# Optimization experiments

Hardware: AMD Instinct MI355X
Metric: run time of the kernel (lower is better)

Reference implementation:

```python
import jax, jax.numpy as jnp
import numpy as np

C = 343.0      # speed of sound (init kwarg c)
F = 16         # number of frequency channels (len(omega))
H = 128        # MLP hidden width
N = 131072     # collocation points


def _mlp(coords, W1, b1, W2, b2, W3, b3):
    # coords: [..., 3] -> [..., 2F] (first F = real part, last F = imag part)
    h = jnp.tanh(coords @ W1 + b1)
    h = jnp.tanh(h @ W2 + b2)
    return h @ W3 + b3


def setup_inputs() -> dict:
    key = jax.random.key(0)
    ks = jax.random.split(key, 4)
    inputs = jax.random.normal(ks[0], (N, 3), dtype=jnp.float32)
    # omega = 2*pi*f for f = 100..1600 Hz (matches init kwarg list)
    omega = 2.0 * jnp.pi * 100.0 * jnp.arange(1, F + 1, dtype=jnp.float32)
    s_in = 1.0 / np.sqrt(3.0)
    s_h = 1.0 / np.sqrt(float(H))
    W1 = jax.random.normal(ks[1], (3, H), dtype=jnp.float32) * s_in
    b1 = jnp.zeros((H,), dtype=jnp.float32)
    W2 = jax.random.normal(ks[2], (H, H), dtype=jnp.float32) * s_h
    b2 = jnp.zeros((H,), dtype=jnp.float32)
    W3 = jax.random.normal(ks[3], (H, 2 * F), dtype=jnp.float32) * s_h
    b3 = jnp.zeros((2 * F,), dtype=jnp.float32)
    return {"inputs": inputs, "omega": omega, "W1": W1, "b1": b1,
            "W2": W2, "b2": b2, "W3": W3, "b3": b3}


def reference(inputs, omega, W1, b1, W2, b2, W3, b3):
    # Pointwise network R^3 -> R^{2F} (real/imag stacked).
    f = lambda c3: _mlp(c3, W1, b1, W2, b2, W3, b3)

    # u: complex pressure per point per frequency, [N, F]
    out = _mlp(inputs, W1, b1, W2, b2, W3, b3)           # [N, 2F]
    u = out[:, :F] + 1j * out[:, F:]

    # Full spatial Hessian per point via forward-over-reverse AD (fused
    # replacement for the torch per-channel autograd.grad loop).
    hess = jax.vmap(jax.jacfwd(jax.jacrev(f)))(inputs)   # [N, 2F, 3, 3]
    lap_ri = jnp.einsum('nfii->nf', hess)                # diagonal trace = Laplacian
    lap = lap_ri[:, :F] + 1j * lap_ri[:, F:]             # [N, F] complex

    # PDE residual skips channel 0, exactly as the torch loop (i+1 indexing).
    k2 = (omega[1:] / C) ** 2                            # [F-1]
    residual = lap[:, 1:] + k2 * u[:, 1:]                # [N, F-1]

    # mean over channels then over batch == global mean of |residual|^2
    return jnp.mean(jnp.abs(residual) ** 2)
```

## Files before the change

kernel.cpp:

```cpp
#include <hip/hip_runtime.h>
#include <math.h>

#ifndef __has_builtin
#define __has_builtin(x) 0
#endif

#define NPTS   131072
#define FCH    16
#define CSND   343.0f
#define PB     16
#define BLOCK  256
#define GRID   512
#define NBLK   (NPTS / PB)

typedef _Float16 half8 __attribute__((ext_vector_type(8)));
typedef _Float16 half2v __attribute__((ext_vector_type(2)));
typedef float    f32x4 __attribute__((ext_vector_type(4)));

static __device__ __forceinline__ unsigned pack2(float a, float b) {
#if __has_builtin(__builtin_amdgcn_cvt_pkrtz)
  return __builtin_bit_cast(unsigned, __builtin_amdgcn_cvt_pkrtz(a, b));
#else
  half2v v; v[0] = (_Float16)a; v[1] = (_Float16)b;
  return __builtin_bit_cast(unsigned, v);
#endif
}

static __device__ __forceinline__ float mytanh(float x) {
  float ax = fabsf(x);
  float e  = __expf(-2.0f * ax);
  float r  = (1.0f - e) * __builtin_amdgcn_rcpf(1.0f + e);
  return copysignf(r, x);
}


__global__ __launch_bounds__(BLOCK, 2) void helmholtz_kernel(
    const float* __restrict__ x,
    const float* __restrict__ omega,
    const float* __restrict__ W1,
    const float* __restrict__ b1,
    const float* __restrict__ W2,
    const float* __restrict__ b2,
    const float* __restrict__ W3,
    const float* __restrict__ b3,
    float* __restrict__ out)
{
  __shared__ unsigned s_A[2][80 * 64];
  __shared__ unsigned s_HG[2][32 * 64];

  const int tid  = threadIdx.x;
  const int w    = tid >> 6;
  const int l    = tid & 63;
  const int col  = l & 15;
  const int quad = l >> 4;

  const int i2 = l;
  const float a0x = W1[2 * i2],     a0y = W1[128 + 2 * i2], a0z = W1[256 + 2 * i2];
  const float a1x = W1[2 * i2 + 1], a1y = W1[129 + 2 * i2], a1z = W1[257 + 2 * i2];
  const float bb0 = b1[2 * i2],     bb1 = b1[2 * i2 + 1];
  const float wsq0 = a0x * a0x + a0y * a0y + a0z * a0z;
  const float wsq1 = a1x * a1x + a1y * a1y + a1z * a1z;

  half8 w2f[2][4];
#pragma unroll
  for (int ntl = 0; ntl < 2; ntl++) {
    const int n = (2 * w + ntl) * 16 + col;
#pragma unroll
    for (int ks = 0; ks < 4; ks++) {
      half8 f;
#pragma unroll
      for (int j = 0; j < 8; j++)
        f[j] = (_Float16)W2[(ks * 32 + (quad << 3) + j) * 128 + n];
      w2f[ntl][ks] = f;
    }
  }
  half8 w3f[4];
  {
    const int n = (w & 1) * 16 + col;
#pragma unroll
    for (int ks = 0; ks < 4; ks++) {
      half8 f;
#pragma unroll
      for (int j = 0; j < 8; j++)
        f[j] = (_Float16)W3[(ks * 32 + (quad << 3) + j) * 32 + n];
      w3f[ks] = f;
    }
  }

  const float b2r0 = b2[2 * w * 16 + col];
  const float b2r1 = b2[(2 * w + 1) * 16 + col];
  float k2v = 0.0f;
  if (col >= 1) {
    float om = omega[col] * (1.0f / CSND);
    k2v = om * om;
  }
  const float b3v = b3[(w & 1) * 16 + col];

  float wsum = 0.0f;

  auto phaseA = [&](int blk, int buf) {
    const int pbase = blk * PB;
    unsigned* sA = s_A[buf];
#pragma unroll
    for (int it = 0; it < 4; it++) {
      int p = w * 4 + it;
      const float* xp = x + (size_t)(pbase + p) * 3;
      float x0 = xp[0], x1 = xp[1], x2 = xp[2];
      float z0 = fmaf(x0, a0x, fmaf(x1, a0y, fmaf(x2, a0z, bb0)));
      float z1 = fmaf(x0, a1x, fmaf(x1, a1y, fmaf(x2, a1z, bb1)));
      float t0 = mytanh(z0), t1 = mytanh(z1);
      float s0 = 1.0f - t0 * t0, s1 = 1.0f - t1 * t1;
      unsigned u_h  = pack2(t0, t1);
      unsigned u_d0 = pack2(s0 * a0x, s1 * a1x);
      unsigned u_d1 = pack2(s0 * a0y, s1 * a1y);
      unsigned u_d2 = pack2(s0 * a0z, s1 * a1z);
      unsigned u_c  = pack2(-2.0f * t0 * s0 * wsq0, -2.0f * t1 * s1 * wsq1);
      int dcol = (((i2 >> 2) ^ p) << 2) + (i2 & 3);
      sA[(p)      * 64 + dcol] = u_h;
      sA[(16 + p) * 64 + dcol] = u_d0;
      sA[(32 + p) * 64 + dcol] = u_d1;
      sA[(48 + p) * 64 + dcol] = u_d2;
      sA[(64 + p) * 64 + dcol] = u_c;
    }
  };

  phaseA(blockIdx.x, 0);
  __syncthreads();

  int parity = 0;
  for (int blk = blockIdx.x; blk < NBLK; blk += gridDim.x, parity ^= 1) {
    int nblk = blk + (int)gridDim.x;
    if (nblk < NBLK) phaseA(nblk, parity ^ 1);

    const unsigned* sA = s_A[parity];
    f32x4 acc[5][2];
#pragma unroll
    for (int mt = 0; mt < 5; mt++)
#pragma unroll
      for (int ntl = 0; ntl < 2; ntl++)
        acc[mt][ntl] = (f32x4){0.0f, 0.0f, 0.0f, 0.0f};

#pragma unroll
    for (int mt = 0; mt < 5; mt++) {
      int m = mt * 16 + col;
#pragma unroll
      for (int ks = 0; ks < 4; ks++) {
        int c = (ks * 4 + quad) ^ col;
        half8 af = *(const half8*)&sA[m * 64 + (c << 2)];
        acc[mt][0] = __builtin_amdgcn_mfma_f32_16x16x32_f16(af, w2f[0][ks], acc[mt][0], 0, 0, 0);
        acc[mt][1] = __builtin_amdgcn_mfma_f32_16x16x32_f16(af, w2f[1][ks], acc[mt][1], 0, 0, 0);
      }
    }

    {
      _Float16* hg = (_Float16*)s_HG[parity];
#pragma unroll
      for (int ntl = 0; ntl < 2; ntl++) {
        int j = (2 * w + ntl) * 16 + col;
        int chunkj = j >> 3;
        float b2v = ntl ? b2r1 : b2r0;
#pragma unroll
        for (int r = 0; r < 4; r++) {
          int p = quad * 4 + r;
          float z2 = acc[0][ntl][r] + b2v;
          float d0 = acc[1][ntl][r], d1 = acc[2][ntl][r], d2 = acc[3][ntl][r];
          float Av = acc[4][ntl][r];
          float t2 = mytanh(z2);
          float s2 = 1.0f - t2 * t2;
          float g  = s2 * (Av - 2.0f * t2 * (d0 * d0 + d1 * d1 + d2 * d2));
          int base = ((chunkj ^ p) << 3) + (j & 7);
          hg[p * 128 + base]        = (_Float16)t2;
          hg[(16 + p) * 128 + base] = (_Float16)g;
        }
      }
    }
    __syncthreads();

    if (w < 2) {
      const unsigned* hgb = s_HG[parity];
      f32x4 dy = (f32x4){0.0f, 0.0f, 0.0f, 0.0f};
      f32x4 dl = (f32x4){0.0f, 0.0f, 0.0f, 0.0f};
#pragma unroll
      for (int ks = 0; ks < 4; ks++) {
        int ca = (ks * 4 + quad) ^ col;
        half8 afy = *(const half8*)&hgb[(col)      * 64 + (ca << 2)];
        half8 afl = *(const half8*)&hgb[(16 + col) * 64 + (ca << 2)];
        dy = __builtin_amdgcn_mfma_f32_16x16x32_f16(afy, w3f[ks], dy, 0, 0, 0);
        dl = __builtin_amdgcn_mfma_f32_16x16x32_f16(afl, w3f[ks], dl, 0, 0, 0);
      }
      if (col >= 1) {
#pragma unroll
        for (int r = 0; r < 4; r++) {
          float yv  = dy[r] + b3v;
          float res = fmaf(k2v, yv, dl[r]);
          wsum += res * res;
        }
      }
    }
  }

#pragma unroll
  for (int off = 32; off > 0; off >>= 1)
    wsum += __shfl_down(wsum, off, 64);
  if (l == 0)
    atomicAdd(out, wsum * (1.0f / ((float)NPTS * (float)(FCH - 1))));
}

extern "C" void kernel_launch(void* const* d_in, const int* in_sizes, int n_in,
                              void* d_out, int out_size, void* d_ws, size_t ws_size,
                              hipStream_t stream) {
  const float* x     = (const float*)d_in[0];
  const float* omega = (const float*)d_in[1];
  const float* W1    = (const float*)d_in[2];
  const float* b1    = (const float*)d_in[3];
  const float* W2    = (const float*)d_in[4];
  const float* b2    = (const float*)d_in[5];
  const float* W3    = (const float*)d_in[6];
  const float* b3    = (const float*)d_in[7];
  float* out = (float*)d_out;

  (void)hipMemsetAsync(out, 0, sizeof(float), stream);
  helmholtz_kernel<<<GRID, BLOCK, 0, stream>>>(x, omega, W1, b1, W2, b2, W3, b3, out);
}
```

Before: 123.9 us.

## Defer output-layer MFMA a step, remap layer-1 threads, and simplify tanh

The final-layer MFMA and residual reduction now run for the previous block at the start of the next iteration, so waves 0-1 no longer stall the whole block after the barrier. That stage overlaps with the other waves' work. Layer-1 now gives each thread one point and eight hidden units, writing 128-bit vectorized LDS stores instead of scattered 32-bit ones. tanh becomes a single exp2 plus reciprocal without abs/copysign, which can overflow to inf for large inputs; the formula then still gives ±1, but the fp accuracy changes.

```diff
diff --git a/kernel.cpp b/kernel.cpp
--- a/kernel.cpp
+++ b/kernel.cpp
@@ -27,10 +27,12 @@
 }
 
 static __device__ __forceinline__ float mytanh(float x) {
-  float ax = fabsf(x);
-  float e  = __expf(-2.0f * ax);
-  float r  = (1.0f - e) * __builtin_amdgcn_rcpf(1.0f + e);
-  return copysignf(r, x);
+#if __has_builtin(__builtin_amdgcn_exp2f)
+  float e = __builtin_amdgcn_exp2f(2.885390082f * x);
+#else
+  float e = __expf(2.0f * x);
+#endif
+  return fmaf(-2.0f, __builtin_amdgcn_rcpf(e + 1.0f), 1.0f);
 }
 
 
@@ -54,12 +56,16 @@
   const int col  = l & 15;
   const int quad = l >> 4;
 
-  const int i2 = l;
-  const float a0x = W1[2 * i2],     a0y = W1[128 + 2 * i2], a0z = W1[256 + 2 * i2];
-  const float a1x = W1[2 * i2 + 1], a1y = W1[129 + 2 * i2], a1z = W1[257 + 2 * i2];
-  const float bb0 = b1[2 * i2],     bb1 = b1[2 * i2 + 1];
-  const float wsq0 = a0x * a0x + a0y * a0y + a0z * a0z;
-  const float wsq1 = a1x * a1x + a1y * a1y + a1z * a1z;
+  const int pA = tid >> 4;
+  const int g  = tid & 15;
+  float wx[8], wy[8], wz[8], bB[8], wq[8];
+#pragma unroll
+  for (int u = 0; u < 8; u++) {
+    int unit = 8 * g + u;
+    wx[u] = W1[unit]; wy[u] = W1[128 + unit]; wz[u] = W1[256 + unit];
+    bB[u] = b1[unit];
+    wq[u] = wx[u] * wx[u] + wy[u] * wy[u] + wz[u] * wz[u];
+  }
 
   half8 w2f[2][4];
 #pragma unroll
@@ -99,28 +105,57 @@
   float wsum = 0.0f;
 
   auto phaseA = [&](int blk, int buf) {
-    const int pbase = blk * PB;
+    const float* xp = x + (size_t)(blk * PB + pA) * 3;
+    float x0 = xp[0], x1 = xp[1], x2 = xp[2];
+    float t[8], s[8];
+#pragma unroll
+    for (int u = 0; u < 8; u++) {
+      float z = fmaf(x0, wx[u], fmaf(x1, wy[u], fmaf(x2, wz[u], bB[u])));
+      t[u] = mytanh(z);
+      s[u] = 1.0f - t[u] * t[u];
+    }
     unsigned* sA = s_A[buf];
-#pragma unroll
-    for (int it = 0; it < 4; it++) {
-      int p = w * 4 + it;
-      const float* xp = x + (size_t)(pbase + p) * 3;
-      float x0 = xp[0], x1 = xp[1], x2 = xp[2];
-      float z0 = fmaf(x0, a0x, fmaf(x1, a0y, fmaf(x2, a0z, bb0)));
-      float z1 = fmaf(x0, a1x, fmaf(x1, a1y, fmaf(x2, a1z, bb1)));
-      float t0 = mytanh(z0), t1 = mytanh(z1);
-      float s0 = 1.0f - t0 * t0, s1 = 1.0f - t1 * t1;
-      unsigned u_h  = pack2(t0, t1);
-      unsigned u_d0 = pack2(s0 * a0x, s1 * a1x);
-      unsigned u_d1 = pack2(s0 * a0y, s1 * a1y);
-      unsigned u_d2 = pack2(s0 * a0z, s1 * a1z);
-      unsigned u_c  = pack2(-2.0f * t0 * s0 * wsq0, -2.0f * t1 * s1 * wsq1);
-      int dcol = (((i2 >> 2) ^ p) << 2) + (i2 & 3);
-      sA[(p)      * 64 + dcol] = u_h;
-      sA[(16 + p) * 64 + dcol] = u_d0;
-      sA[(32 + p) * 64 + dcol] = u_d1;
-      sA[(48 + p) * 64 + dcol] = u_d2;
-      sA[(64 + p) * 64 + dcol] = u_c;
+    const int base = (g ^ pA) << 2;
+    uint4 q;
+    q = make_uint4(pack2(t[0], t[1]), pack2(t[2], t[3]),
+                   pack2(t[4], t[5]), pack2(t[6], t[7]));
+    *(uint4*)&sA[(pA)      * 64 + base] = q;
+    q = make_uint4(pack2(s[0] * wx[0], s[1] * wx[1]), pack2(s[2] * wx[2], s[3] * wx[3]),
+                   pack2(s[4] * wx[4], s[5] * wx[5]), pack2(s[6] * wx[6], s[7] * wx[7]));
+    *(uint4*)&sA[(16 + pA) * 64 + base] = q;
+    q = make_uint4(pack2(s[0] * wy[0], s[1] * wy[1]), pack2(s[2] * wy[2], s[3] * wy[3]),
+                   pack2(s[4] * wy[4], s[5] * wy[5]), pack2(s[6] * wy[6], s[7] * wy[7]));
+    *(uint4*)&sA[(32 + pA) * 64 + base] = q;
+    q = make_uint4(pack2(s[0] * wz[0], s[1] * wz[1]), pack2(s[2] * wz[2], s[3] * wz[3]),
+                   pack2(s[4] * wz[4], s[5] * wz[5]), pack2(s[6] * wz[6], s[7] * wz[7]));
+    *(uint4*)&sA[(48 + pA) * 64 + base] = q;
+    float c[8];
+#pragma unroll
+    for (int u = 0; u < 8; u++) c[u] = -2.0f * t[u] * s[u] * wq[u];
+    q = make_uint4(pack2(c[0], c[1]), pack2(c[2], c[3]),
+                   pack2(c[4], c[5]), pack2(c[6], c[7]));
+    *(uint4*)&sA[(64 + pA) * 64 + base] = q;
+  };
+
+  auto phaseDE = [&](int buf) {
+    const unsigned* hgb = s_HG[buf];
+    f32x4 dy = (f32x4){0.0f, 0.0f, 0.0f, 0.0f};
+    f32x4 dl = (f32x4){0.0f, 0.0f, 0.0f, 0.0f};
+#pragma unroll
+    for (int ks = 0; ks < 4; ks++) {
+      int ca = (ks * 4 + quad) ^ col;
+      half8 afy = *(const half8*)&hgb[(col)      * 64 + (ca << 2)];
+      half8 afl = *(const half8*)&hgb[(16 + col) * 64 + (ca << 2)];
+      dy = __builtin_amdgcn_mfma_f32_16x16x32_f16(afy, w3f[ks], dy, 0, 0, 0);
+      dl = __builtin_amdgcn_mfma_f32_16x16x32_f16(afl, w3f[ks], dl, 0, 0, 0);
+    }
+    if (col >= 1) {
+#pragma unroll
+      for (int r = 0; r < 4; r++) {
+        float yv  = dy[r] + b3v;
+        float res = fmaf(k2v, yv, dl[r]);
+        wsum += res * res;
+      }
     }
   };
 
@@ -129,6 +164,8 @@
 
   int parity = 0;
   for (int blk = blockIdx.x; blk < NBLK; blk += gridDim.x, parity ^= 1) {
+    if (w < 2 && blk != (int)blockIdx.x) phaseDE(parity ^ 1);
+
     int nblk = blk + (int)gridDim.x;
     if (nblk < NBLK) phaseA(nblk, parity ^ 1);
 
@@ -167,37 +204,17 @@
           float Av = acc[4][ntl][r];
           float t2 = mytanh(z2);
           float s2 = 1.0f - t2 * t2;
-          float g  = s2 * (Av - 2.0f * t2 * (d0 * d0 + d1 * d1 + d2 * d2));
+          float gg = s2 * (Av - 2.0f * t2 * (d0 * d0 + d1 * d1 + d2 * d2));
           int base = ((chunkj ^ p) << 3) + (j & 7);
           hg[p * 128 + base]        = (_Float16)t2;
-          hg[(16 + p) * 128 + base] = (_Float16)g;
+          hg[(16 + p) * 128 + base] = (_Float16)gg;
         }
       }
     }
     __syncthreads();
-
-    if (w < 2) {
-      const unsigned* hgb = s_HG[parity];
-      f32x4 dy = (f32x4){0.0f, 0.0f, 0.0f, 0.0f};
-      f32x4 dl = (f32x4){0.0f, 0.0f, 0.0f, 0.0f};
-#pragma unroll
-      for (int ks = 0; ks < 4; ks++) {
-        int ca = (ks * 4 + quad) ^ col;
-        half8 afy = *(const half8*)&hgb[(col)      * 64 + (ca << 2)];
-        half8 afl = *(const half8*)&hgb[(16 + col) * 64 + (ca << 2)];
-        dy = __builtin_amdgcn_mfma_f32_16x16x32_f16(afy, w3f[ks], dy, 0, 0, 0);
-        dl = __builtin_amdgcn_mfma_f32_16x16x32_f16(afl, w3f[ks], dl, 0, 0, 0);
-      }
-      if (col >= 1) {
-#pragma unroll
-        for (int r = 0; r < 4; r++) {
-          float yv  = dy[r] + b3v;
-          float res = fmaf(k2v, yv, dl[r]);
-          wsum += res * res;
-        }
-      }
-    }
-  }
+  }
+
+  if (w < 2) phaseDE(parity ^ 1);
 
 #pragma unroll
   for (int off = 32; off > 0; off >>= 1)
```

Result: faster. 121.4 us (-2.0%).
